# Optimization experiments

Hardware: AMD Instinct MI355X
Metric: run time of the kernel (lower is better)

The kernel has to match this reference:

```python
import jax, jax.numpy as jnp
import numpy as np

B, Y = 1024, 50000
MAX_TRIALS = 4096


def setup_inputs() -> dict:
    key = jax.random.key(0)
    k1, k2 = jax.random.split(key)
    input_ = jax.random.normal(k1, (B, Y), dtype=jnp.float32)
    pos = jax.random.randint(k2, (B,), 0, Y)
    target = jnp.zeros((B, Y), jnp.float32).at[jnp.arange(B), pos].set(1.0)
    return {"input_": input_, "target": target, "max_num_trials": MAX_TRIALS}


def reference(input_, target, max_num_trials):
    """WARP loss. The torch original sequentially samples negatives WITHOUT
    replacement per row until margin 1 + s_neg - s_pos >= 0 or max_num_trials
    is hit. Sampling without replacement == taking a uniform random
    permutation of the negative labels and scanning it; the first violating
    position t gives num_trials = t+1. This lets us fully vectorize the
    irregular loop while computing identical math (up to RNG stream)."""
    Bn, Yn = input_.shape
    rows = jnp.arange(Bn)
    pos = jnp.argmax(target, axis=1)                 # one positive per row (as J[i,1])
    pos_score = input_[rows, pos]                    # [B]

    # uniform random permutation of the Y-1 negatives per row:
    # random sort keys, force the positive label to sort last, drop it.
    u = jax.random.uniform(jax.random.key(42), (Bn, Yn))
    u = u.at[rows, pos].set(2.0)
    perm = jnp.argsort(u, axis=1)[:, : Yn - 1]       # [B, Y-1] negative label ids

    neg_scores = jnp.take_along_axis(input_, perm, axis=1)   # [B, Y-1]
    margins = 1.0 + neg_scores - pos_score[:, None]
    trial_ok = jnp.arange(Yn - 1)[None, :] < max_num_trials
    viol = (margins >= 0.0) & trial_ok
    found = jnp.any(viol, axis=1)
    first = jnp.argmax(viol, axis=1)                 # first violating trial index
    num_trials = (first + 1).astype(jnp.float32)
    # loss_weight = log(floor((Y-1)/num_trials)); 0 when no violator found
    L = jnp.where(found, jnp.log(jnp.floor((Yn - 1.0) / num_trials)), 0.0)
    neg_score = jnp.where(
        found, jnp.take_along_axis(neg_scores, first[:, None], axis=1)[:, 0], 0.0
    )
    loss = L * (1.0 - pos_score + neg_score)         # [B]
    return jnp.sum(loss, keepdims=True)              # shape (1,), as torch.sum(dim=0, keepdim=True)
```

## Files before the change

### kernel.cpp

```cpp
#include <hip/hip_runtime.h>
#include <stdint.h>

#define BN 1024
#define YN 50000
#define SEGS 8
#define SEGLEN 6250
#define CAP 192

#define TF_ROUND(r) { x0 += x1; x1 = (x1 << (r)) | (x1 >> (32 - (r))); x1 ^= x0; }

__device__ __forceinline__ uint32_t tf_bits(uint32_t ctr) {
    const uint32_t ks0 = 0u;
    const uint32_t ks1 = 42u;
    const uint32_t ks2 = 0x1BD11BDAu ^ 0u ^ 42u;
    uint32_t x1 = ctr + ks1;
    uint32_t x0 = x1;
    x1 = ((x1 << 13) | (x1 >> 19)) ^ x0;
    TF_ROUND(15) TF_ROUND(26) TF_ROUND(6)
    x0 += ks1; x1 += ks2 + 1u;
    TF_ROUND(17) TF_ROUND(29) TF_ROUND(16) TF_ROUND(24)
    x0 += ks2; x1 += ks0 + 2u;
    TF_ROUND(13) TF_ROUND(15) TF_ROUND(26) TF_ROUND(6)
    x0 += ks0; x1 += ks1 + 3u;
    TF_ROUND(17) TF_ROUND(29) TF_ROUND(16) TF_ROUND(24)
    x0 += ks1; x1 += ks2 + 4u;
    TF_ROUND(13) TF_ROUND(15) TF_ROUND(26) TF_ROUND(6)
    x0 += ks2; x1 += ks0 + 5u;
    return x0 ^ x1;
}

struct WS {
    uint32_t* cnt; int* flag; int* pos; float* ps; float* row_loss; uint32_t* cand;
};
static inline WS ws_layout(void* d_ws) {
    uint32_t* p = (uint32_t*)d_ws;
    WS w;
    w.cnt = p; w.flag = (int*)(p + BN); w.pos = (int*)(p + 2 * BN);
    w.ps = (float*)(p + 3 * BN); w.row_loss = (float*)(p + 4 * BN);
    w.cand = p + 5 * BN;
    return w;
}

__global__ __launch_bounds__(256) void gen_kernel(
    const float* __restrict__ input, const float* __restrict__ target,
    uint32_t* __restrict__ cnt, uint32_t* __restrict__ cand,
    int* __restrict__ pos_out, float* __restrict__ ps_out)
{
    const int tid = threadIdx.x;
    if (blockIdx.x < BN) {
        const int row = blockIdx.x;
        const size_t base = (size_t)row * YN;
        __shared__ volatile int s_pos;
        if (tid == 0) s_pos = -1;
        __syncthreads();
        const float4* t4 = (const float4*)(target + base);
        for (int j4 = tid; j4 < YN / 4; j4 += 256) {
            if (s_pos >= 0) break;
            float4 v = t4[j4];
            int c0 = 4 * j4;
            if (v.x != 0.0f) s_pos = c0;
            if (v.y != 0.0f) s_pos = c0 + 1;
            if (v.z != 0.0f) s_pos = c0 + 2;
            if (v.w != 0.0f) s_pos = c0 + 3;
        }
        __syncthreads();
        if (tid == 0) {
            int p = s_pos;
            pos_out[row] = p;
            ps_out[row] = input[base + p];
        }
        return;
    }
    const int b = blockIdx.x - BN;
    const int row = b >> 3;
    const int seg = b & 7;
    const uint32_t base32 = (uint32_t)row * YN;
    const int start = seg * SEGLEN;
    const int end = start + SEGLEN;
    uint32_t* mycnt = cnt + row;
    uint32_t* mycand = cand + row * CAP;
    uint32_t ctr = base32 + (uint32_t)(start + tid);
    for (int col = start + tid; col < end; col += 256, ctr += 256u) {
        uint32_t bits = tf_bits(ctr);
        if (bits < (1u << 23)) {
            uint32_t idx = atomicAdd(mycnt, 1u);
            if (idx < CAP) mycand[idx] = ((bits >> 9) << 17) | (uint32_t)col;
        }
    }
}

__global__ __launch_bounds__(256) void resolve_kernel(
    const float* __restrict__ input, const uint32_t* __restrict__ cnt,
    const uint32_t* __restrict__ cand, const int* __restrict__ pos_,
    const float* __restrict__ ps_, const int* __restrict__ mt_ptr,
    float* __restrict__ row_loss, int* __restrict__ flag)
{
    const int gtid = blockIdx.x * 256 + threadIdx.x;
    const int row = gtid >> 6;
    const int lane = gtid & 63;
    const uint32_t n = cnt[row];
    if (n > CAP) { if (lane == 0) flag[row] = 1; return; }
    const int pos = pos_[row];
    const float ps = ps_[row];
    const uint32_t* cl = cand + row * CAP;
    const float* rowp = input + (size_t)row * YN;

    uint32_t mk = 0xFFFFFFFFu;
    for (uint32_t i = lane; i < n; i += 64) {
        uint32_t e = cl[i];
        int col = (int)(e & 0x1FFFFu);
        if (col == pos) continue;
        float s = rowp[col];
        if ((1.0f + s) - ps >= 0.0f) mk = (e < mk) ? e : mk;
    }
    for (int off = 32; off > 0; off >>= 1) {
        uint32_t o = (uint32_t)__shfl_xor((int)mk, off, 64);
        mk = (o < mk) ? o : mk;
    }
    if (mk == 0xFFFFFFFFu) {
        if (lane == 0) flag[row] = 1;
        return;
    }
    uint32_t c = 0;
    for (uint32_t i = lane; i < n; i += 64) {
        uint32_t e = cl[i];
        int col = (int)(e & 0x1FFFFu);
        c += ((e < mk) && (col != pos)) ? 1u : 0u;
    }
    for (int off = 32; off > 0; off >>= 1) c += (uint32_t)__shfl_xor((int)c, off, 64);
    if (lane == 0) {
        uint32_t rank = c;
        float loss = 0.0f;
        if (rank < (uint32_t)mt_ptr[0]) {
            int cstar = (int)(mk & 0x1FFFFu);
            float ns = rowp[cstar];
            float nt = (float)(rank + 1u);
            loss = logf(floorf(49999.0f / nt)) * ((1.0f - ps) + ns);
        }
        row_loss[row] = loss;
    }
}

__global__ __launch_bounds__(256) void fallback_kernel(
    const float* __restrict__ input, const int* __restrict__ flag,
    const int* __restrict__ pos_, const float* __restrict__ ps_,
    const int* __restrict__ mt_ptr, float* __restrict__ row_loss)
{
    const int row = blockIdx.x;
    if (!flag[row]) return;
    const int tid = threadIdx.x;
    const int pos = pos_[row];
    const float ps = ps_[row];
    const uint32_t base32 = (uint32_t)row * YN;
    const float* rowp = input + (size_t)row * YN;

    __shared__ uint64_t smin[256];
    __shared__ uint32_t ssum[256];

    uint64_t mk = ~0ull;
    for (int col = tid; col < YN; col += 256) {
        uint32_t bits = tf_bits(base32 + (uint32_t)col);
        uint64_t key = ((uint64_t)(bits >> 9) << 17) | (uint32_t)col;
        float m = (1.0f + rowp[col]) - ps;
        if ((m >= 0.0f) && (col != pos) && (key < mk)) mk = key;
    }
    smin[tid] = mk;
    __syncthreads();
    for (int s = 128; s > 0; s >>= 1) {
        if (tid < s) { uint64_t o = smin[tid + s]; if (o < smin[tid]) smin[tid] = o; }
        __syncthreads();
    }
    const uint64_t kstar = smin[0];
    if (kstar == ~0ull) {
        if (tid == 0) row_loss[row] = 0.0f;
        return;
    }
    uint32_t c = 0;
    for (int col = tid; col < YN; col += 256) {
        uint32_t bits = tf_bits(base32 + (uint32_t)col);
        uint64_t key = ((uint64_t)(bits >> 9) << 17) | (uint32_t)col;
        c += ((key < kstar) && (col != pos)) ? 1u : 0u;
    }
    ssum[tid] = c;
    __syncthreads();
    for (int s = 128; s > 0; s >>= 1) {
        if (tid < s) ssum[tid] += ssum[tid + s];
        __syncthreads();
    }
    if (tid == 0) {
        uint32_t rank = ssum[0];
        float loss = 0.0f;
        if (rank < (uint32_t)mt_ptr[0]) {
            int cstar = (int)(kstar & 0x1FFFFull);
            float ns = rowp[cstar];
            float nt = (float)(rank + 1u);
            loss = logf(floorf(49999.0f / nt)) * ((1.0f - ps) + ns);
        }
        row_loss[row] = loss;
    }
}

__global__ __launch_bounds__(256) void reduce_kernel(
    const float* __restrict__ row_loss, float* __restrict__ out)
{
    __shared__ float s[256];
    int tid = threadIdx.x;
    float acc = 0.0f;
    for (int i = tid; i < BN; i += 256) acc += row_loss[i];
    s[tid] = acc;
    __syncthreads();
    for (int st = 128; st > 0; st >>= 1) {
        if (tid < st) s[tid] += s[tid + st];
        __syncthreads();
    }
    if (tid == 0) out[0] = s[0];
}

extern "C" void kernel_launch(void* const* d_in, const int* in_sizes, int n_in,
                              void* d_out, int out_size, void* d_ws, size_t ws_size,
                              hipStream_t stream) {
    const float* input  = (const float*)d_in[0];
    const float* target = (const float*)d_in[1];
    const int*   mt     = (const int*)d_in[2];
    float* out = (float*)d_out;
    WS w = ws_layout(d_ws);

    hipMemsetAsync(d_ws, 0, 2 * BN * sizeof(uint32_t), stream);

    gen_kernel<<<BN + BN * SEGS, 256, 0, stream>>>(
        input, target, w.cnt, w.cand, w.pos, w.ps);
    resolve_kernel<<<BN / 4, 256, 0, stream>>>(
        input, w.cnt, w.cand, w.pos, w.ps, mt, w.row_loss, w.flag);
    fallback_kernel<<<BN, 256, 0, stream>>>(
        input, w.flag, w.pos, w.ps, mt, w.row_loss);
    reduce_kernel<<<1, 256, 0, stream>>>(w.row_loss, out);
}
```

Before: 457.7 us.

## Fuse resolve, fallback and reduce into one kernel; unroll Threefry generation loop

Resolve, fallback and the final reduction are merged into a single finish kernel. The fallback runs per wavefront inside it, and a last-block-done atomic counter performs the global sum, which removes two kernel launches. The candidate generation loop is unrolled by two so each thread computes two Threefry hashes per iteration, giving more instruction-level parallelism. The trade-off is that any row that needs the fallback now scans all 50000 columns with a single 64-lane wave instead of a 256-thread block, so those rows become slow if they occur.

```diff
diff --git a/kernel.cpp b/kernel.cpp
--- a/kernel.cpp
+++ b/kernel.cpp
@@ -30,12 +30,12 @@
 }
 
 struct WS {
-    uint32_t* cnt; int* flag; int* pos; float* ps; float* row_loss; uint32_t* cand;
+    uint32_t* cnt; uint32_t* done; int* pos; float* ps; float* row_loss; uint32_t* cand;
 };
 static inline WS ws_layout(void* d_ws) {
     uint32_t* p = (uint32_t*)d_ws;
     WS w;
-    w.cnt = p; w.flag = (int*)(p + BN); w.pos = (int*)(p + 2 * BN);
+    w.cnt = p; w.done = p + BN; w.pos = (int*)(p + 2 * BN);
     w.ps = (float*)(p + 3 * BN); w.row_loss = (float*)(p + 4 * BN);
     w.cand = p + 5 * BN;
     return w;
@@ -79,8 +79,21 @@
     const int end = start + SEGLEN;
     uint32_t* mycnt = cnt + row;
     uint32_t* mycand = cand + row * CAP;
-    uint32_t ctr = base32 + (uint32_t)(start + tid);
-    for (int col = start + tid; col < end; col += 256, ctr += 256u) {
+    int col = start + tid;
+    uint32_t ctr = base32 + (uint32_t)col;
+    for (; col + 256 < end; col += 512, ctr += 512u) {
+        uint32_t bits0 = tf_bits(ctr);
+        uint32_t bits1 = tf_bits(ctr + 256u);
+        if (bits0 < (1u << 23)) {
+            uint32_t idx = atomicAdd(mycnt, 1u);
+            if (idx < CAP) mycand[idx] = ((bits0 >> 9) << 17) | (uint32_t)col;
+        }
+        if (bits1 < (1u << 23)) {
+            uint32_t idx = atomicAdd(mycnt, 1u);
+            if (idx < CAP) mycand[idx] = ((bits1 >> 9) << 17) | (uint32_t)(col + 256);
+        }
+    }
+    if (col < end) {
         uint32_t bits = tf_bits(ctr);
         if (bits < (1u << 23)) {
             uint32_t idx = atomicAdd(mycnt, 1u);
@@ -89,131 +102,108 @@
     }
 }
 
-__global__ __launch_bounds__(256) void resolve_kernel(
+__global__ __launch_bounds__(256) void finish_kernel(
     const float* __restrict__ input, const uint32_t* __restrict__ cnt,
     const uint32_t* __restrict__ cand, const int* __restrict__ pos_,
     const float* __restrict__ ps_, const int* __restrict__ mt_ptr,
-    float* __restrict__ row_loss, int* __restrict__ flag)
+    float* __restrict__ row_loss, uint32_t* __restrict__ done,
+    float* __restrict__ out)
 {
-    const int gtid = blockIdx.x * 256 + threadIdx.x;
-    const int row = gtid >> 6;
-    const int lane = gtid & 63;
-    const uint32_t n = cnt[row];
-    if (n > CAP) { if (lane == 0) flag[row] = 1; return; }
+    const int tid = threadIdx.x;
+    const int lane = tid & 63;
+    const int row = blockIdx.x * 4 + (tid >> 6);
     const int pos = pos_[row];
     const float ps = ps_[row];
-    const uint32_t* cl = cand + row * CAP;
     const float* rowp = input + (size_t)row * YN;
-
-    uint32_t mk = 0xFFFFFFFFu;
-    for (uint32_t i = lane; i < n; i += 64) {
-        uint32_t e = cl[i];
-        int col = (int)(e & 0x1FFFFu);
-        if (col == pos) continue;
-        float s = rowp[col];
-        if ((1.0f + s) - ps >= 0.0f) mk = (e < mk) ? e : mk;
-    }
-    for (int off = 32; off > 0; off >>= 1) {
-        uint32_t o = (uint32_t)__shfl_xor((int)mk, off, 64);
-        mk = (o < mk) ? o : mk;
-    }
-    if (mk == 0xFFFFFFFFu) {
-        if (lane == 0) flag[row] = 1;
-        return;
-    }
-    uint32_t c = 0;
-    for (uint32_t i = lane; i < n; i += 64) {
-        uint32_t e = cl[i];
-        int col = (int)(e & 0x1FFFFu);
-        c += ((e < mk) && (col != pos)) ? 1u : 0u;
-    }
-    for (int off = 32; off > 0; off >>= 1) c += (uint32_t)__shfl_xor((int)c, off, 64);
-    if (lane == 0) {
-        uint32_t rank = c;
-        float loss = 0.0f;
-        if (rank < (uint32_t)mt_ptr[0]) {
-            int cstar = (int)(mk & 0x1FFFFu);
-            float ns = rowp[cstar];
-            float nt = (float)(rank + 1u);
-            loss = logf(floorf(49999.0f / nt)) * ((1.0f - ps) + ns);
-        }
-        row_loss[row] = loss;
-    }
-}
-
-__global__ __launch_bounds__(256) void fallback_kernel(
-    const float* __restrict__ input, const int* __restrict__ flag,
-    const int* __restrict__ pos_, const float* __restrict__ ps_,
-    const int* __restrict__ mt_ptr, float* __restrict__ row_loss)
-{
-    const int row = blockIdx.x;
-    if (!flag[row]) return;
-    const int tid = threadIdx.x;
-    const int pos = pos_[row];
-    const float ps = ps_[row];
-    const uint32_t base32 = (uint32_t)row * YN;
-    const float* rowp = input + (size_t)row * YN;
-
-    __shared__ uint64_t smin[256];
-    __shared__ uint32_t ssum[256];
-
-    uint64_t mk = ~0ull;
-    for (int col = tid; col < YN; col += 256) {
-        uint32_t bits = tf_bits(base32 + (uint32_t)col);
-        uint64_t key = ((uint64_t)(bits >> 9) << 17) | (uint32_t)col;
-        float m = (1.0f + rowp[col]) - ps;
-        if ((m >= 0.0f) && (col != pos) && (key < mk)) mk = key;
-    }
-    smin[tid] = mk;
+    const uint32_t n = cnt[row];
+    const uint32_t mt = (uint32_t)mt_ptr[0];
+    float loss = 0.0f;
+    bool need_fallback = (n > CAP);
+
+    if (!need_fallback) {
+        const uint32_t* cl = cand + row * CAP;
+        uint32_t mk = 0xFFFFFFFFu;
+        for (uint32_t i = lane; i < n; i += 64) {
+            uint32_t e = cl[i];
+            int col = (int)(e & 0x1FFFFu);
+            if (col != pos) {
+                float s = rowp[col];
+                if ((1.0f + s) - ps >= 0.0f) mk = (e < mk) ? e : mk;
+            }
+        }
+        for (int off = 32; off > 0; off >>= 1) {
+            uint32_t o = (uint32_t)__shfl_xor((int)mk, off, 64);
+            mk = (o < mk) ? o : mk;
+        }
+        if (mk == 0xFFFFFFFFu) {
+            need_fallback = true;
+        } else {
+            uint32_t c = 0;
+            for (uint32_t i = lane; i < n; i += 64) {
+                uint32_t e = cl[i];
+                int col = (int)(e & 0x1FFFFu);
+                c += ((e < mk) && (col != pos)) ? 1u : 0u;
+            }
+            for (int off = 32; off > 0; off >>= 1)
+                c += (uint32_t)__shfl_xor((int)c, off, 64);
+            if (c < mt) {
+                int cstar = (int)(mk & 0x1FFFFu);
+                float ns = rowp[cstar];
+                float nt = (float)(c + 1u);
+                loss = logf(floorf(49999.0f / nt)) * ((1.0f - ps) + ns);
+            }
+        }
+    }
+    if (need_fallback) {
+        const uint32_t base32 = (uint32_t)row * YN;
+        uint64_t mk = ~0ull;
+        for (int col = lane; col < YN; col += 64) {
+            uint32_t bits = tf_bits(base32 + (uint32_t)col);
+            uint64_t key = ((uint64_t)(bits >> 9) << 17) | (uint32_t)col;
+            float m = (1.0f + rowp[col]) - ps;
+            if ((m >= 0.0f) && (col != pos) && (key < mk)) mk = key;
+        }
+        for (int off = 32; off > 0; off >>= 1) {
+            uint64_t o = (uint64_t)__shfl_xor((long long)mk, off, 64);
+            mk = (o < mk) ? o : mk;
+        }
+        if (mk != ~0ull) {
+            uint32_t c = 0;
+            for (int col = lane; col < YN; col += 64) {
+                uint32_t bits = tf_bits(base32 + (uint32_t)col);
+                uint64_t key = ((uint64_t)(bits >> 9) << 17) | (uint32_t)col;
+                c += ((key < mk) && (col != pos)) ? 1u : 0u;
+            }
+            for (int off = 32; off > 0; off >>= 1)
+                c += (uint32_t)__shfl_xor((int)c, off, 64);
+            if (c < mt) {
+                int cstar = (int)(mk & 0x1FFFFull);
+                float ns = rowp[cstar];
+                float nt = (float)(c + 1u);
+                loss = logf(floorf(49999.0f / nt)) * ((1.0f - ps) + ns);
+            }
+        }
+    }
+    if (lane == 0) row_loss[row] = loss;
+
+    __threadfence();
     __syncthreads();
-    for (int s = 128; s > 0; s >>= 1) {
-        if (tid < s) { uint64_t o = smin[tid + s]; if (o < smin[tid]) smin[tid] = o; }
+    __shared__ bool s_last;
+    if (tid == 0) s_last = (atomicAdd(done, 1u) == (uint32_t)(gridDim.x - 1));
+    __syncthreads();
+    if (s_last) {
+        __threadfence();
+        __shared__ float s[256];
+        float acc = 0.0f;
+        for (int i = tid; i < BN; i += 256) acc += row_loss[i];
+        s[tid] = acc;
         __syncthreads();
-    }
-    const uint64_t kstar = smin[0];
-    if (kstar == ~0ull) {
-        if (tid == 0) row_loss[row] = 0.0f;
-        return;
-    }
-    uint32_t c = 0;
-    for (int col = tid; col < YN; col += 256) {
-        uint32_t bits = tf_bits(base32 + (uint32_t)col);
-        uint64_t key = ((uint64_t)(bits >> 9) << 17) | (uint32_t)col;
-        c += ((key < kstar) && (col != pos)) ? 1u : 0u;
-    }
-    ssum[tid] = c;
-    __syncthreads();
-    for (int s = 128; s > 0; s >>= 1) {
-        if (tid < s) ssum[tid] += ssum[tid + s];
-        __syncthreads();
-    }
-    if (tid == 0) {
-        uint32_t rank = ssum[0];
-        float loss = 0.0f;
-        if (rank < (uint32_t)mt_ptr[0]) {
-            int cstar = (int)(kstar & 0x1FFFFull);
-            float ns = rowp[cstar];
-            float nt = (float)(rank + 1u);
-            loss = logf(floorf(49999.0f / nt)) * ((1.0f - ps) + ns);
-        }
-        row_loss[row] = loss;
-    }
-}
-
-__global__ __launch_bounds__(256) void reduce_kernel(
-    const float* __restrict__ row_loss, float* __restrict__ out)
-{
-    __shared__ float s[256];
-    int tid = threadIdx.x;
-    float acc = 0.0f;
-    for (int i = tid; i < BN; i += 256) acc += row_loss[i];
-    s[tid] = acc;
-    __syncthreads();
-    for (int st = 128; st > 0; st >>= 1) {
-        if (tid < st) s[tid] += s[tid + st];
-        __syncthreads();
-    }
-    if (tid == 0) out[0] = s[0];
+        for (int st = 128; st > 0; st >>= 1) {
+            if (tid < st) s[tid] += s[tid + st];
+            __syncthreads();
+        }
+        if (tid == 0) out[0] = s[0];
+    }
 }
 
 extern "C" void kernel_launch(void* const* d_in, const int* in_sizes, int n_in,
@@ -229,9 +219,6 @@
 
     gen_kernel<<<BN + BN * SEGS, 256, 0, stream>>>(
         input, target, w.cnt, w.cand, w.pos, w.ps);
-    resolve_kernel<<<BN / 4, 256, 0, stream>>>(
-        input, w.cnt, w.cand, w.pos, w.ps, mt, w.row_loss, w.flag);
-    fallback_kernel<<<BN, 256, 0, stream>>>(
-        input, w.flag, w.pos, w.ps, mt, w.row_loss);
-    reduce_kernel<<<1, 256, 0, stream>>>(w.row_loss, out);
-}
+    finish_kernel<<<BN / 4, 256, 0, stream>>>(
+        input, w.cnt, w.cand, w.pos, w.ps, mt, w.row_loss, w.done, out);
+}
```

Measured after the change: 470.7 us. 2.8% more time.
